# Kernel tuning notes

Measured on AMD Instinct MI355X. Metric: run time of the kernel, lower is better.

Reference implementation:

```python
import jax, jax.numpy as jnp
import numpy as np

D_MODEL = 1024
N_HEADS = 16
D_HEAD = D_MODEL // N_HEADS  # 64
SCALE = 1.0 / float(np.sqrt(D_HEAD))


def setup_inputs() -> dict:
    key = jax.random.key(0)
    kx, kq, kk, kv, ko = jax.random.split(key, 5)
    B, L = 1, 4096
    x = jax.random.normal(kx, (B, L, D_MODEL), dtype=jnp.float32)
    init = 0.02  # small init so softmax isn't saturated
    Wq = jax.random.normal(kq, (D_MODEL, D_MODEL), dtype=jnp.float32) * init
    Wk = jax.random.normal(kk, (D_MODEL, D_MODEL), dtype=jnp.float32) * init
    Wv = jax.random.normal(kv, (D_MODEL, D_MODEL), dtype=jnp.float32) * init
    Wo = jax.random.normal(ko, (D_MODEL, D_MODEL), dtype=jnp.float32) * init
    return {"x": x, "Wq": Wq, "Wk": Wk, "Wv": Wv, "Wo": Wo}


def reference(x, Wq, Wk, Wv, Wo):
    # x: [B, L, d_model]; torch Linear (no bias): y = x @ W.T
    B, L, _ = x.shape

    def split_heads(t):  # [B, L, d_model] -> [B, H, L, Dh]
        return t.reshape(B, L, N_HEADS, D_HEAD).transpose(0, 2, 1, 3)

    q = split_heads(x @ Wq.T)
    k = split_heads(x @ Wk.T)
    v = split_heads(x @ Wv.T)

    # Full (non-flash) attention: explicit [B, H, L, L] scores (causal=False, eval dropout=0)
    scores = jnp.einsum("bhld,bhmd->bhlm", q, k) * SCALE
    attn = jax.nn.softmax(scores, axis=-1)
    out = jnp.einsum("bhlm,bhmd->bhld", attn, v)

    out = out.transpose(0, 2, 1, 3).reshape(B, L, D_MODEL)
    return out @ Wo.T
```

## Files before the change

### kernel.cpp

```cpp
#include <hip/hip_runtime.h>

typedef _Float16 f16_t;
typedef __fp16 fp16x2 __attribute__((ext_vector_type(2)));
typedef _Float16 f16x2 __attribute__((ext_vector_type(2)));
typedef _Float16 f16x4 __attribute__((ext_vector_type(4)));
typedef _Float16 f16x8 __attribute__((ext_vector_type(8)));
typedef float f32x4 __attribute__((ext_vector_type(4)));

#define D_MODEL 1024
#define LSEQ 4096
#define NH 16
#define DH 64
#define QSCALE 0.18033688011112042f

#define GLDS16(g, l)                                                     \
    __builtin_amdgcn_global_load_lds(                                    \
        (const __attribute__((address_space(1))) void*)(g),              \
        (__attribute__((address_space(3))) void*)(l), 16, 0, 0)

#define WAIT_VM(n) asm volatile("s_waitcnt vmcnt(" #n ")" ::: "memory")

__global__ __launch_bounds__(256) void cvt_x(const float* __restrict__ in,
                                             f16_t* __restrict__ out, int n) {
    int i = (blockIdx.x * 256 + threadIdx.x) * 4;
    if (i + 3 < n) {
        float4 v = *(const float4*)&in[i];
        alignas(8) f16_t o4[4] = {(f16_t)v.x, (f16_t)v.y, (f16_t)v.z, (f16_t)v.w};
        *(uint2*)&out[i] = *(const uint2*)o4;
    }
}

__global__ __launch_bounds__(256) void cvt_w4(const float* __restrict__ w0,
                                              const float* __restrict__ w1,
                                              const float* __restrict__ w2,
                                              const float* __restrict__ w3,
                                              f16_t* __restrict__ out) {
    const int q = blockIdx.y;
    const float* src = (q == 0) ? w0 : (q == 1) ? w1 : (q == 2) ? w2 : w3;
    const float scale = (q == 0) ? QSCALE : 1.f;
    int i = (blockIdx.x * 256 + threadIdx.x) * 4;
    float4 v = *(const float4*)&src[i];
    alignas(8) f16_t o4[4] = {(f16_t)(v.x * scale), (f16_t)(v.y * scale),
                              (f16_t)(v.z * scale), (f16_t)(v.w * scale)};
    *(uint2*)&out[(size_t)q * (D_MODEL * D_MODEL) + i] = *(const uint2*)o4;
}

__global__ __launch_bounds__(256, 3) void gemm_f16(const f16_t* __restrict__ A,
                                                   const f16_t* __restrict__ B,
                                                   void* __restrict__ Cout,
                                                   int M, int N, int K, int mode) {
    __shared__ alignas(16) f16_t As[3][128 * 32];
    __shared__ alignas(16) f16_t Bs[3][128 * 32];

    const int tid  = threadIdx.x;
    const int wave = tid >> 6;
    const int lane = tid & 63;
    const int quad = lane >> 4;
    const int l16  = lane & 15;
    const int wm = (wave & 1) * 64;
    const int wn = (wave >> 1) * 64;
    const int bm = blockIdx.x * 128;
    const int bn = blockIdx.y * 128;

    f32x4 acc[4][4] = {};
    const int nk = K / 32;

    auto stage = [&](int kt, int b) {
        const int c0 = wave * 2;
        GLDS16(&A[(size_t)(bm + c0 * 16 + l16) * K + kt * 32 + quad * 8],
               &As[b][c0 * 512]);
        GLDS16(&A[(size_t)(bm + (c0 + 1) * 16 + l16) * K + kt * 32 + quad * 8],
               &As[b][(c0 + 1) * 512]);
        GLDS16(&B[(size_t)(bn + c0 * 16 + l16) * K + kt * 32 + quad * 8],
               &Bs[b][c0 * 512]);
        GLDS16(&B[(size_t)(bn + (c0 + 1) * 16 + l16) * K + kt * 32 + quad * 8],
               &Bs[b][(c0 + 1) * 512]);
    };

    stage(0, 0);
    stage(1, 1);
    for (int kt = 0; kt < nk; ++kt) {
        const int cb = kt % 3;
        if (kt < nk - 1) WAIT_VM(4);
        else             WAIT_VM(0);
        __syncthreads();
        if (kt + 2 < nk) stage(kt + 2, (kt + 2) % 3);

        f16x8 af[4], bfr[4];
#pragma unroll
        for (int mt = 0; mt < 4; ++mt)
            af[mt] = *(const f16x8*)&As[cb][((wm >> 4) + mt) * 512 + lane * 8];
#pragma unroll
        for (int nt = 0; nt < 4; ++nt)
            bfr[nt] = *(const f16x8*)&Bs[cb][((wn >> 4) + nt) * 512 + lane * 8];
#pragma unroll
        for (int mt = 0; mt < 4; ++mt)
#pragma unroll
            for (int nt = 0; nt < 4; ++nt)
                acc[mt][nt] = __builtin_amdgcn_mfma_f32_16x16x32_f16(
                    bfr[nt], af[mt], acc[mt][nt], 0, 0, 0);
    }

#pragma unroll
    for (int mt = 0; mt < 4; ++mt)
#pragma unroll
        for (int nt = 0; nt < 4; ++nt) {
            int row = bm + wm + mt * 16 + l16;
            int col = bn + wn + nt * 16 + quad * 4;
            if (mode == 0) {
                f16x4 p = {(f16_t)acc[mt][nt][0], (f16_t)acc[mt][nt][1],
                           (f16_t)acc[mt][nt][2], (f16_t)acc[mt][nt][3]};
                *(f16x4*)&((f16_t*)Cout)[((size_t)(col >> 6) * M + row) * 64 +
                                         (col & 63)] = p;
            } else {
                *(f32x4*)&((float*)Cout)[(size_t)row * N + col] = acc[mt][nt];
            }
        }
}

__global__ __launch_bounds__(256) void transpose_v(const f16_t* __restrict__ vh,
                                                   f16_t* __restrict__ v4) {
    __shared__ f16_t Ts[64][72];
    const int t = threadIdx.x;
    const int lt = blockIdx.x;
    const int head = blockIdx.y;

#pragma unroll
    for (int i = 0; i < 2; ++i) {
        int idx = t + i * 256;
        int row = idx >> 3, part = idx & 7;
        *(uint4*)&Ts[row][part * 8] =
            *(const uint4*)&vh[((size_t)head * LSEQ + lt * 64 + row) * DH + part * 8];
    }
    __syncthreads();

    const int c8  = t >> 5;
    const int mtp = c8 >> 2, dt = c8 & 3;
    const int l0  = (t & 31) * 2;
    alignas(16) f16_t buf[16];
#pragma unroll
    for (int li = 0; li < 2; ++li) {
        const int l = l0 + li;
        const int g = l >> 4, l16 = l & 15;
#pragma unroll
        for (int j = 0; j < 8; ++j) {
            int key = mtp * 32 + (j < 4 ? 4 * g + j : 16 + 4 * g + (j - 4));
            buf[li * 8 + j] = Ts[key][dt * 16 + l16];
        }
    }
    f16_t* dst = v4 + (size_t)head * (LSEQ * DH) + (size_t)lt * 4096 + c8 * 512 + l0 * 8;
    *(uint4*)&dst[0] = *(const uint4*)&buf[0];
    *(uint4*)&dst[8] = *(const uint4*)&buf[8];
}

__global__ __launch_bounds__(512, 2) void attn_kernel(const f16_t* __restrict__ qh,
                                                      const f16_t* __restrict__ kh,
                                                      const f16_t* __restrict__ v4,
                                                      f16_t* __restrict__ ao) {
    __shared__ alignas(16) f16_t smem[32768];
    __shared__ alignas(16) float lscr[16 * 64];
    f16_t* KsB = smem;
    f16_t* VsB = smem + 16384;

    const int tid  = threadIdx.x;
    const int wave = tid >> 6;
    const int lane = tid & 63;
    const int quad = lane >> 4;
    const int l16  = lane & 15;
    const int wq   = wave & 3;
    const int kha  = wave >> 2;

    const int id = blockIdx.x;
    const int head = id & 15;
    const int qrow0 = (id >> 4) * 256 + wq * 64;

    const f16_t* Q  = qh + (size_t)head * LSEQ * DH;
    const f16_t* K  = kh + (size_t)head * LSEQ * DH;
    const f16_t* V4 = v4 + (size_t)head * (LSEQ * DH);

    f16x8 qf[4][2];
#pragma unroll
    for (int qt = 0; qt < 4; ++qt)
#pragma unroll
        for (int kc = 0; kc < 2; ++kc)
            qf[qt][kc] = *(const f16x8*)
                &Q[(size_t)(qrow0 + qt * 16 + l16) * DH + kc * 32 + quad * 8];

    f32x4 o[4][4] = {};
    float lp[4] = {0.f, 0.f, 0.f, 0.f};

    auto stage = [&](int kt, int b) {
        f16_t* ks = KsB + (kha * 2 + b) * 4096;
        f16_t* vs = VsB + (kha * 2 + b) * 4096;
        const int ktg = kha * 32 + kt;
#pragma unroll
        for (int jj = 0; jj < 2; ++jj) {
            const int j = wq * 2 + jj;
            GLDS16(&K[(size_t)(ktg * 64 + wq * 16 + l16) * DH + jj * 32 + quad * 8],
                   &ks[j * 512]);
            GLDS16(&V4[(size_t)ktg * 4096 + wq * 1024 + jj * 512 + lane * 8],
                   &vs[wq * 1024 + jj * 512]);
        }
    };

    const int NT = LSEQ / 2 / 64;
    stage(0, 0);
    for (int kt = 0; kt < NT; ++kt) {
        const int cb = kt & 1;
        WAIT_VM(0);
        __syncthreads();
        if (kt + 1 < NT) stage(kt + 1, cb ^ 1);

        const f16_t* ks = KsB + (kha * 2 + cb) * 4096;
        const f16_t* vs = VsB + (kha * 2 + cb) * 4096;

#pragma unroll
        for (int mtp = 0; mtp < 2; ++mtp) {
            f32x4 s[2][4] = {};
#pragma unroll
            for (int h = 0; h < 2; ++h) {
                const int mt = mtp * 2 + h;
                f16x8 kf0 = *(const f16x8*)&ks[(mt * 2 + 0) * 512 + lane * 8];
                f16x8 kf1 = *(const f16x8*)&ks[(mt * 2 + 1) * 512 + lane * 8];
#pragma unroll
                for (int qt = 0; qt < 4; ++qt) {
                    s[h][qt] = __builtin_amdgcn_mfma_f32_16x16x32_f16(
                        kf0, qf[qt][0], s[h][qt], 0, 0, 0);
                    s[h][qt] = __builtin_amdgcn_mfma_f32_16x16x32_f16(
                        kf1, qf[qt][1], s[h][qt], 0, 0, 0);
                }
            }

            f16x8 vfd[4];
#pragma unroll
            for (int dt = 0; dt < 4; ++dt)
                vfd[dt] = *(const f16x8*)&vs[(mtp * 4 + dt) * 512 + lane * 8];

#pragma unroll
            for (int qt = 0; qt < 4; ++qt) {
                float e0 = __builtin_amdgcn_exp2f(s[0][qt][0]);
                float e1 = __builtin_amdgcn_exp2f(s[0][qt][1]);
                float e2 = __builtin_amdgcn_exp2f(s[0][qt][2]);
                float e3 = __builtin_amdgcn_exp2f(s[0][qt][3]);
                float e4 = __builtin_amdgcn_exp2f(s[1][qt][0]);
                float e5 = __builtin_amdgcn_exp2f(s[1][qt][1]);
                float e6 = __builtin_amdgcn_exp2f(s[1][qt][2]);
                float e7 = __builtin_amdgcn_exp2f(s[1][qt][3]);
                lp[qt] += ((e0 + e1) + (e2 + e3)) + ((e4 + e5) + (e6 + e7));
                fp16x2 p01 = __builtin_amdgcn_cvt_pkrtz(e0, e1);
                fp16x2 p23 = __builtin_amdgcn_cvt_pkrtz(e2, e3);
                fp16x2 p45 = __builtin_amdgcn_cvt_pkrtz(e4, e5);
                fp16x2 p67 = __builtin_amdgcn_cvt_pkrtz(e6, e7);
                f16x8 p = {__builtin_bit_cast(f16x2, p01)[0],
                           __builtin_bit_cast(f16x2, p01)[1],
                           __builtin_bit_cast(f16x2, p23)[0],
                           __builtin_bit_cast(f16x2, p23)[1],
                           __builtin_bit_cast(f16x2, p45)[0],
                           __builtin_bit_cast(f16x2, p45)[1],
                           __builtin_bit_cast(f16x2, p67)[0],
                           __builtin_bit_cast(f16x2, p67)[1]};
#pragma unroll
                for (int dt = 0; dt < 4; ++dt)
                    o[dt][qt] = __builtin_amdgcn_mfma_f32_16x16x32_f16(
                        vfd[dt], p, o[dt][qt], 0, 0, 0);
            }
        }
    }

    __syncthreads();
    float* scr = (float*)smem;
    if (wave >= 4) {
#pragma unroll
        for (int dt = 0; dt < 4; ++dt)
#pragma unroll
            for (int qt = 0; qt < 4; ++qt)
                *(f32x4*)&scr[(((wave - 4) * 16 + dt * 4 + qt) * 64 + lane) * 4] =
                    o[dt][qt];
#pragma unroll
        for (int qt = 0; qt < 4; ++qt)
            lscr[((wave - 4) * 4 + qt) * 64 + lane] = lp[qt];
    }
    __syncthreads();
    if (wave < 4) {
#pragma unroll
        for (int dt = 0; dt < 4; ++dt)
#pragma unroll
            for (int qt = 0; qt < 4; ++qt)
                o[dt][qt] += *(const f32x4*)
                    &scr[((wave * 16 + dt * 4 + qt) * 64 + lane) * 4];
#pragma unroll
        for (int qt = 0; qt < 4; ++qt) {
            float t = lp[qt] + lscr[(wave * 4 + qt) * 64 + lane];
            t += __shfl_xor(t, 16, 64);
            t += __shfl_xor(t, 32, 64);
            lp[qt] = 1.f / t;
        }
#pragma unroll
        for (int dt = 0; dt < 4; ++dt)
#pragma unroll
            for (int qt = 0; qt < 4; ++qt) {
                f16x4 ov = {(f16_t)(o[dt][qt][0] * lp[qt]),
                            (f16_t)(o[dt][qt][1] * lp[qt]),
                            (f16_t)(o[dt][qt][2] * lp[qt]),
                            (f16_t)(o[dt][qt][3] * lp[qt])};
                int qrow = qrow0 + qt * 16 + l16;
                *(f16x4*)&ao[(size_t)qrow * D_MODEL + head * 64 + dt * 16 +
                             quad * 4] = ov;
            }
    }
}

extern "C" void kernel_launch(void* const* d_in, const int* in_sizes, int n_in,
                              void* d_out, int out_size, void* d_ws, size_t ws_size,
                              hipStream_t stream) {
    const float* x  = (const float*)d_in[0];
    const float* Wq = (const float*)d_in[1];
    const float* Wk = (const float*)d_in[2];
    const float* Wv = (const float*)d_in[3];
    const float* Wo = (const float*)d_in[4];

    f16_t* xb = (f16_t*)d_ws;
    f16_t* wq = xb + (size_t)LSEQ * D_MODEL;
    f16_t* wo = wq + (size_t)3 * D_MODEL * D_MODEL;
    f16_t* qh = wo + (size_t)D_MODEL * D_MODEL;
    f16_t* kh = qh + (size_t)LSEQ * D_MODEL;
    f16_t* vh = kh + (size_t)LSEQ * D_MODEL;
    f16_t* v4 = vh + (size_t)LSEQ * D_MODEL;
    f16_t* ao = v4 + (size_t)LSEQ * D_MODEL;

    const int nx = LSEQ * D_MODEL;
    cvt_x<<<nx / 1024, 256, 0, stream>>>(x, xb, nx);
    cvt_w4<<<dim3(D_MODEL * D_MODEL / 1024, 4), 256, 0, stream>>>(Wq, Wk, Wv, Wo, wq);

    gemm_f16<<<dim3(LSEQ / 128, 3 * D_MODEL / 128), 256, 0, stream>>>(
        xb, wq, qh, LSEQ, 3 * D_MODEL, D_MODEL, 0);

    transpose_v<<<dim3(LSEQ / 64, NH), 256, 0, stream>>>(vh, v4);

    attn_kernel<<<dim3((LSEQ / 256) * NH), 512, 0, stream>>>(qh, kh, v4, ao);

    gemm_f16<<<dim3(LSEQ / 128, D_MODEL / 128), 256, 0, stream>>>(
        ao, wo, d_out, LSEQ, D_MODEL, D_MODEL, 1);
}
```

Measured before the change: 249.7 us.

## Give each wave private K LDS buffers and load V directly to registers

Each wave now stages its own K tiles into a private double-buffered LDS region and reads V fragments straight from global memory into registers. This removes the per-iteration block-wide __syncthreads. The cost is that every wave reloads the same K and V tiles, which multiplies global and L2 traffic. LDS use also grows to 128 KB, which likely cuts occupancy from two blocks per CU to one, and V global-load latency is exposed within the iteration.

```diff
diff --git a/kernel.cpp b/kernel.cpp
--- a/kernel.cpp
+++ b/kernel.cpp
@@ -157,11 +157,8 @@
                                                       const f16_t* __restrict__ kh,
                                                       const f16_t* __restrict__ v4,
                                                       f16_t* __restrict__ ao) {
-    __shared__ alignas(16) f16_t smem[32768];
+    __shared__ alignas(16) f16_t Ksm[8 * 8192];
     __shared__ alignas(16) float lscr[16 * 64];
-    f16_t* KsB = smem;
-    f16_t* VsB = smem + 16384;
-
     const int tid  = threadIdx.x;
     const int wave = tid >> 6;
     const int lane = tid & 63;
@@ -174,9 +171,10 @@
     const int head = id & 15;
     const int qrow0 = (id >> 4) * 256 + wq * 64;
 
-    const f16_t* Q  = qh + (size_t)head * LSEQ * DH;
-    const f16_t* K  = kh + (size_t)head * LSEQ * DH;
-    const f16_t* V4 = v4 + (size_t)head * (LSEQ * DH);
+    const f16_t* Q   = qh + (size_t)head * LSEQ * DH;
+    const f16_t* K   = kh + (size_t)head * LSEQ * DH + (size_t)kha * (LSEQ / 2) * DH;
+    const f16_t* V4h = v4 + (size_t)head * LSEQ * DH + (size_t)kha * (LSEQ / 2) * DH;
+    f16_t* kpriv = Ksm + wave * 8192;
 
     f16x8 qf[4][2];
 #pragma unroll
@@ -189,52 +187,51 @@
     f32x4 o[4][4] = {};
     float lp[4] = {0.f, 0.f, 0.f, 0.f};
 
-    auto stage = [&](int kt, int b) {
-        f16_t* ks = KsB + (kha * 2 + b) * 4096;
-        f16_t* vs = VsB + (kha * 2 + b) * 4096;
-        const int ktg = kha * 32 + kt;
-#pragma unroll
-        for (int jj = 0; jj < 2; ++jj) {
-            const int j = wq * 2 + jj;
-            GLDS16(&K[(size_t)(ktg * 64 + wq * 16 + l16) * DH + jj * 32 + quad * 8],
-                   &ks[j * 512]);
-            GLDS16(&V4[(size_t)ktg * 4096 + wq * 1024 + jj * 512 + lane * 8],
-                   &vs[wq * 1024 + jj * 512]);
-        }
-    };
+#pragma unroll
+    for (int c = 0; c < 8; ++c)
+        GLDS16(&K[(size_t)((c >> 1) * 16 + l16) * DH + (c & 1) * 32 + quad * 8],
+               &kpriv[c * 512]);
 
     const int NT = LSEQ / 2 / 64;
-    stage(0, 0);
     for (int kt = 0; kt < NT; ++kt) {
         const int cb = kt & 1;
+        const f16_t* ks = kpriv + cb * 4096;
+
         WAIT_VM(0);
-        __syncthreads();
-        if (kt + 1 < NT) stage(kt + 1, cb ^ 1);
-
-        const f16_t* ks = KsB + (kha * 2 + cb) * 4096;
-        const f16_t* vs = VsB + (kha * 2 + cb) * 4096;
+
+        f16x8 vf[8];
+#pragma unroll
+        for (int c = 0; c < 8; ++c)
+            vf[c] = *(const f16x8*)&V4h[(size_t)kt * 4096 + c * 512 + lane * 8];
+        __builtin_amdgcn_sched_barrier(0);
+
+        if (kt + 1 < NT) {
+            const f16_t* kn = K + (size_t)(kt + 1) * 64 * DH;
+            f16_t* kd = kpriv + (cb ^ 1) * 4096;
+#pragma unroll
+            for (int c = 0; c < 8; ++c)
+                GLDS16(&kn[(size_t)((c >> 1) * 16 + l16) * DH + (c & 1) * 32 + quad * 8],
+                       &kd[c * 512]);
+        }
 
 #pragma unroll
         for (int mtp = 0; mtp < 2; ++mtp) {
+            f16x8 kf[4];
+#pragma unroll
+            for (int c = 0; c < 4; ++c)
+                kf[c] = *(const f16x8*)&ks[(mtp * 4 + c) * 512 + lane * 8];
+
             f32x4 s[2][4] = {};
 #pragma unroll
             for (int h = 0; h < 2; ++h) {
-                const int mt = mtp * 2 + h;
-                f16x8 kf0 = *(const f16x8*)&ks[(mt * 2 + 0) * 512 + lane * 8];
-                f16x8 kf1 = *(const f16x8*)&ks[(mt * 2 + 1) * 512 + lane * 8];
 #pragma unroll
                 for (int qt = 0; qt < 4; ++qt) {
                     s[h][qt] = __builtin_amdgcn_mfma_f32_16x16x32_f16(
-                        kf0, qf[qt][0], s[h][qt], 0, 0, 0);
+                        kf[h * 2 + 0], qf[qt][0], s[h][qt], 0, 0, 0);
                     s[h][qt] = __builtin_amdgcn_mfma_f32_16x16x32_f16(
-                        kf1, qf[qt][1], s[h][qt], 0, 0, 0);
+                        kf[h * 2 + 1], qf[qt][1], s[h][qt], 0, 0, 0);
                 }
             }
-
-            f16x8 vfd[4];
-#pragma unroll
-            for (int dt = 0; dt < 4; ++dt)
-                vfd[dt] = *(const f16x8*)&vs[(mtp * 4 + dt) * 512 + lane * 8];
 
 #pragma unroll
             for (int qt = 0; qt < 4; ++qt) {
@@ -262,13 +259,14 @@
 #pragma unroll
                 for (int dt = 0; dt < 4; ++dt)
                     o[dt][qt] = __builtin_amdgcn_mfma_f32_16x16x32_f16(
-                        vfd[dt], p, o[dt][qt], 0, 0, 0);
+                        vf[mtp * 4 + dt], p, o[dt][qt], 0, 0, 0);
             }
         }
     }
 
+    WAIT_VM(0);
     __syncthreads();
-    float* scr = (float*)smem;
+    float* scr = (float*)Ksm;
     if (wave >= 4) {
 #pragma unroll
         for (int dt = 0; dt < 4; ++dt)
```

Result: slower. 255.1 us (+2.2%).
